# Kernel optimization log

Measured on AMD Instinct MI355X. Metric: run time of the kernel, lower is better.

The kernel has to match this reference:

```python
import jax, jax.numpy as jnp
import numpy as np

AGENT = 0
TAU = 0.5
EPS = 1e-10


def setup_inputs() -> dict:
    key = jax.random.key(0)
    ks = jax.random.split(key, 8)
    B, A, L, D, AD, OUT = 32768, 6, 225, 128, 64, 5
    E = A - 1  # 5 visible entities
    return {
        "observation": jax.random.normal(ks[0], (B, A, L), dtype=jnp.float32),
        "enc_w": jax.random.normal(ks[1], (L, D), dtype=jnp.float32) * 0.05,
        "enc_b": jnp.zeros((D,), dtype=jnp.float32),
        "q_w": jax.random.normal(ks[2], (D, AD), dtype=jnp.float32) * 0.05,
        "k_w": jax.random.normal(ks[3], (D, AD), dtype=jnp.float32) * 0.05,
        "fc_w": jax.random.normal(ks[4], (2 * E * D, OUT), dtype=jnp.float32) * 0.05,
        "fc_b": jnp.zeros((OUT,), dtype=jnp.float32),
        "u": jax.random.uniform(ks[5], (B, OUT), dtype=jnp.float32),
    }


def reference(observation, enc_w, enc_b, q_w, k_w, fc_w, fc_b, u):
    B, A, L = observation.shape
    others = np.array([i for i in range(A) if i != AGENT])  # static index list
    vis_obs = observation[:, others]          # (B, E, L)
    ag_obs = observation[:, AGENT:AGENT + 1]  # (B, 1, L)

    # ObservationEncoder: Linear + ReLU (shared weights)
    ag_e = jax.nn.relu(ag_obs @ enc_w + enc_b)    # (B, 1, D)
    vis_e = jax.nn.relu(vis_obs @ enc_w + enc_b)  # (B, E, D)

    # EntityAttention: scaled dot-product, softmax over entities
    q = ag_e @ q_w   # (B, 1, AD)
    k = vis_e @ k_w  # (B, E, AD)
    scores = jnp.einsum('bqa,bea->be', q, k) / jnp.sqrt(jnp.asarray(q.shape[-1], q.dtype))
    alphas = jax.nn.softmax(scores, axis=-1)  # (B, E)

    # attention-weighted per-entity encodings
    weighted = alphas[..., None] * vis_e                      # (B, E, D)
    agent_rep = jnp.broadcast_to(ag_e, weighted.shape)        # (B, E, D)
    concat = jnp.concatenate([agent_rep, weighted], axis=-2)  # (B, 2E, D)
    flat = concat.reshape(B, -1)                              # (B, 2*E*D)

    logits = flat @ fc_w + fc_b  # (B, OUT)

    # gumbel_softmax(tau=0.5, hard=False)
    g = -jnp.log(-jnp.log(u + EPS) + EPS)
    probs = jax.nn.softmax((logits + g) / TAU, axis=1)
    predicted_actions = jnp.argmax(probs, axis=1, keepdims=True)  # (B, 1) int
    return predicted_actions
```

## Files before the change

kernel.cpp:

```cpp
#include <hip/hip_runtime.h>
#include <math.h>

#define NB   32768
#define AG   6
#define LL   225
#define DD   128
#define EE   5
#define NOUT 5
#define ADIM 64

#define WS_M        0
#define WS_W1T      16384
#define WS_F2T      17024
#define WS_BSWZ_B   80896

#define SBLK 16
#define ENC_STRIDE 132
#define LDS_FLOATS 12672

typedef __attribute__((ext_vector_type(8))) short short8v;
typedef __attribute__((ext_vector_type(4))) float float4v;

__device__ __forceinline__ unsigned short bf_hi(float x, float* rem) {
    unsigned u = __float_as_uint(x);
    unsigned r = (u + 0x7FFFu + ((u >> 16) & 1u)) & 0xFFFF0000u;
    *rem = x - __uint_as_float(r);
    return (unsigned short)(r >> 16);
}

struct Tri { unsigned h, m, l; };
__device__ __forceinline__ Tri split2(float x0, float x1) {
    Tri t;
    unsigned u0 = __float_as_uint(x0), u1 = __float_as_uint(x1);
    t.h = __builtin_amdgcn_perm(u1, u0, 0x07060302u);
    float r0 = x0 - __uint_as_float(u0 & 0xFFFF0000u);
    float r1 = x1 - __uint_as_float(u1 & 0xFFFF0000u);
    unsigned v0 = __float_as_uint(r0), v1 = __float_as_uint(r1);
    t.m = __builtin_amdgcn_perm(v1, v0, 0x07060302u);
    float q0 = r0 - __uint_as_float(v0 & 0xFFFF0000u);
    float q1 = r1 - __uint_as_float(v1 & 0xFFFF0000u);
    t.l = __builtin_amdgcn_perm(__float_as_uint(q1), __float_as_uint(q0), 0x07060302u);
    return t;
}

__device__ __forceinline__ void stage8(unsigned short* aswz, const float* obs_blk,
                                       int slot, int k0) {
    const int r  = slot >> 3;
    const int k8 = slot & 7;
    const int k  = k0 + 8 * k8;
    float4 v0 = make_float4(0.f, 0.f, 0.f, 0.f);
    float4 v1 = make_float4(0.f, 0.f, 0.f, 0.f);
    if (k + 7 <= 224) {
        v0 = *(const float4*)&obs_blk[r * LL + k];
        v1 = *(const float4*)&obs_blk[r * LL + k + 4];
    } else if (k == 224) {
        v0.x = obs_blk[r * LL + 224];
    }
    Tri a = split2(v0.x, v0.y);
    Tri b = split2(v0.z, v0.w);
    Tri cc = split2(v1.x, v1.y);
    Tri d = split2(v1.z, v1.w);
    const int mt  = r >> 4, mm = r & 15;
    const int kbL = k8 >> 2;
    const int la  = mm + 16 * (k8 & 3);
    const int pla = la ^ ((la >> 2) & 12);
    unsigned short* p = aswz + ((kbL * 6 + mt) * 3) * 512 + pla * 8;
    *(uint4*)(p)        = make_uint4(a.h, b.h, cc.h, d.h);
    *(uint4*)(p + 512)  = make_uint4(a.m, b.m, cc.m, d.m);
    *(uint4*)(p + 1024) = make_uint4(a.l, b.l, cc.l, d.l);
}

__global__ void precompute_kernel(const float* __restrict__ q_w,
                                  const float* __restrict__ k_w,
                                  const float* __restrict__ enc_w,
                                  const float* __restrict__ fc_w,
                                  float* __restrict__ ws) {
    int b = blockIdx.x;
    int t = threadIdx.x;
    if (b < 128) {
        float s = 0.f;
        #pragma unroll 8
        for (int j = 0; j < ADIM; ++j)
            s = fmaf(q_w[b * ADIM + j], k_w[t * ADIM + j], s);
        ws[WS_M + b * 128 + t] = s * 0.125f;
    } else if (b == 128) {
        int d = t;
        #pragma unroll
        for (int o = 0; o < NOUT; ++o) {
            float s = 0.f;
            #pragma unroll
            for (int e = 0; e < EE; ++e)
                s += fc_w[(e * 128 + d) * NOUT + o];
            ws[WS_W1T + o * 128 + d] = s;
            #pragma unroll
            for (int e = 0; e < EE; ++e)
                ws[WS_F2T + (e * 5 + o) * 128 + d] = fc_w[(640 + e * 128 + d) * NOUT + o];
        }
    } else {
        int idx = (b - 129) * 128 + t;
        int lane = idx & 63;
        int rest = idx >> 6;
        int s    = rest % 3;
        int r2   = rest / 3;
        int nt   = r2 & 7;
        int kb   = r2 >> 3;
        unsigned short* bs = (unsigned short*)((char*)ws + WS_BSWZ_B);
        const int n     = nt * 16 + (lane & 15);
        const int kbase = kb * 32 + (lane >> 4) * 8;
        #pragma unroll
        for (int j = 0; j < 8; ++j) {
            int k = kbase + j;
            float x = (k < LL) ? enc_w[k * DD + n] : 0.f;
            float q1, q2, q3;
            unsigned short h = bf_hi(x,  &q1);
            unsigned short m = bf_hi(q1, &q2);
            unsigned short l = bf_hi(q2, &q3);
            bs[(((kb * 8 + nt) * 3 + s) * 64 + lane) * 8 + j] =
                (s == 0) ? h : (s == 1) ? m : l;
        }
    }
}

__global__ __launch_bounds__(512, 4)
void policy_kernel(const float* __restrict__ obs,
                   const float* __restrict__ enc_b,
                   const float* __restrict__ fc_b,
                   const float* __restrict__ u,
                   const float* __restrict__ ws,
                   int* __restrict__ out) {
    __shared__ float lds[LDS_FLOATS];
    unsigned short* aswz = (unsigned short*)lds;

    const int tid  = threadIdx.x;
    const int lane = tid & 63;
    const int w    = tid >> 6;
    const int wr   = w >> 2;
    const int wc   = w & 3;
    const int bs0  = blockIdx.x * SBLK;
    const float* obs_blk = obs + (size_t)bs0 * (AG * LL);
    const unsigned short* bswz = (const unsigned short*)((const char*)ws + WS_BSWZ_B);
    const int pl8 = (lane ^ ((lane >> 2) & 12)) * 8;

    float4v acc[3][2];
    #pragma unroll
    for (int m3 = 0; m3 < 3; ++m3)
        #pragma unroll
        for (int nt = 0; nt < 2; ++nt)
            acc[m3][nt] = (float4v){0.f, 0.f, 0.f, 0.f};

    #pragma unroll 1
    for (int c = 0; c < 4; ++c) {
        const int k0 = 64 * c;
        stage8(aswz, obs_blk, tid, k0);
        if (tid < 256) stage8(aswz, obs_blk, 512 + tid, k0);
        __syncthreads();

        #pragma unroll
        for (int kbL = 0; kbL < 2; ++kbL) {
            const int kb = 2 * c + kbL;
            short8v Bf[2][3];
            #pragma unroll
            for (int nt = 0; nt < 2; ++nt)
                #pragma unroll
                for (int s = 0; s < 3; ++s)
                    Bf[nt][s] = *(const short8v*)
                        &bswz[(((kb * 8 + (2 * wc + nt)) * 3 + s) * 64 + lane) * 8];
            #pragma unroll
            for (int m3 = 0; m3 < 3; ++m3) {
                const unsigned short* ap =
                    aswz + ((kbL * 6 + (wr * 3 + m3)) * 3) * 512 + pl8;
                short8v Ah = *(const short8v*)(ap);
                short8v Am = *(const short8v*)(ap + 512);
                short8v Al = *(const short8v*)(ap + 1024);
                #pragma unroll
                for (int nt = 0; nt < 2; ++nt) {
                    float4v d = acc[m3][nt];
                    d = __builtin_amdgcn_mfma_f32_16x16x32_bf16(Ah, Bf[nt][0], d, 0, 0, 0);
                    d = __builtin_amdgcn_mfma_f32_16x16x32_bf16(Ah, Bf[nt][1], d, 0, 0, 0);
                    d = __builtin_amdgcn_mfma_f32_16x16x32_bf16(Am, Bf[nt][0], d, 0, 0, 0);
                    d = __builtin_amdgcn_mfma_f32_16x16x32_bf16(Ah, Bf[nt][2], d, 0, 0, 0);
                    d = __builtin_amdgcn_mfma_f32_16x16x32_bf16(Al, Bf[nt][0], d, 0, 0, 0);
                    d = __builtin_amdgcn_mfma_f32_16x16x32_bf16(Am, Bf[nt][1], d, 0, 0, 0);
                    acc[m3][nt] = d;
                }
            }
        }
        __syncthreads();
    }

    {
        #pragma unroll
        for (int nt = 0; nt < 2; ++nt) {
            const int col = (2 * wc + nt) * 16 + (lane & 15);
            const float bb = enc_b[col];
            #pragma unroll
            for (int m3 = 0; m3 < 3; ++m3) {
                const int rbase = (wr * 3 + m3) * 16 + (lane >> 4) * 4;
                #pragma unroll
                for (int reg = 0; reg < 4; ++reg)
                    lds[(rbase + reg) * ENC_STRIDE + col] =
                        fmaxf(acc[m3][nt][reg] + bb, 0.f);
            }
        }
    }
    __syncthreads();

    const float* Mw = ws + WS_M;
    const int c0 = 2 * lane;
    const int sA = 2 * w;
    const int rA = sA * AG;
    const int rB = rA + AG;

    float t0[2] = {0.f, 0.f}, t1[2] = {0.f, 0.f};
    #pragma unroll 4
    for (int d = 0; d < DD; d += 4) {
        float4 a0 = *(const float4*)&lds[rA * ENC_STRIDE + d];
        float4 a1 = *(const float4*)&lds[rB * ENC_STRIDE + d];
        float2 m0 = *(const float2*)&Mw[(size_t)(d + 0) * DD + c0];
        float2 m1 = *(const float2*)&Mw[(size_t)(d + 1) * DD + c0];
        float2 m2 = *(const float2*)&Mw[(size_t)(d + 2) * DD + c0];
        float2 m3 = *(const float2*)&Mw[(size_t)(d + 3) * DD + c0];
        t0[0] = fmaf(a0.x, m0.x, t0[0]); t1[0] = fmaf(a0.x, m0.y, t1[0]);
        t0[0] = fmaf(a0.y, m1.x, t0[0]); t1[0] = fmaf(a0.y, m1.y, t1[0]);
        t0[0] = fmaf(a0.z, m2.x, t0[0]); t1[0] = fmaf(a0.z, m2.y, t1[0]);
        t0[0] = fmaf(a0.w, m3.x, t0[0]); t1[0] = fmaf(a0.w, m3.y, t1[0]);
        t0[1] = fmaf(a1.x, m0.x, t0[1]); t1[1] = fmaf(a1.x, m0.y, t1[1]);
        t0[1] = fmaf(a1.y, m1.x, t0[1]); t1[1] = fmaf(a1.y, m1.y, t1[1]);
        t0[1] = fmaf(a1.z, m2.x, t0[1]); t1[1] = fmaf(a1.z, m2.y, t1[1]);
        t0[1] = fmaf(a1.w, m3.x, t0[1]); t1[1] = fmaf(a1.w, m3.y, t1[1]);
    }

    float vx[2][EE], vy[2][EE], sc[2][EE];
    #pragma unroll
    for (int j = 0; j < 2; ++j)
        #pragma unroll
        for (int e = 0; e < EE; ++e) {
            float2 v = *(const float2*)&lds[((sA + j) * AG + 1 + e) * ENC_STRIDE + c0];
            vx[j][e] = v.x; vy[j][e] = v.y;
            sc[j][e] = t0[j] * v.x + t1[j] * v.y;
        }
    #pragma unroll
    for (int off = 32; off > 0; off >>= 1)
        #pragma unroll
        for (int j = 0; j < 2; ++j)
            #pragma unroll
            for (int e = 0; e < EE; ++e)
                sc[j][e] += __shfl_xor(sc[j][e], off, 64);

    float alpha[2][EE];
    #pragma unroll
    for (int j = 0; j < 2; ++j) {
        float mx = sc[j][0];
        #pragma unroll
        for (int e = 1; e < EE; ++e) mx = fmaxf(mx, sc[j][e]);
        float sum = 0.f;
        #pragma unroll
        for (int e = 0; e < EE; ++e) { alpha[j][e] = expf(sc[j][e] - mx); sum += alpha[j][e]; }
        const float inv = 1.f / sum;
        #pragma unroll
        for (int e = 0; e < EE; ++e) alpha[j][e] *= inv;
    }

    float Lg[2][NOUT];
    #pragma unroll
    for (int j = 0; j < 2; ++j) {
        float2 a2 = *(const float2*)&lds[(sA + j) * AG * ENC_STRIDE + c0];
        #pragma unroll
        for (int o = 0; o < NOUT; ++o) {
            float2 w1 = *(const float2*)&ws[WS_W1T + o * DD + c0];
            Lg[j][o] = fmaf(a2.x, w1.x, a2.y * w1.y);
        }
    }
    #pragma unroll
    for (int e = 0; e < EE; ++e) {
        float wxj[2], wyj[2];
        #pragma unroll
        for (int j = 0; j < 2; ++j) { wxj[j] = alpha[j][e] * vx[j][e]; wyj[j] = alpha[j][e] * vy[j][e]; }
        #pragma unroll
        for (int o = 0; o < NOUT; ++o) {
            float2 f2 = *(const float2*)&ws[WS_F2T + (e * NOUT + o) * DD + c0];
            #pragma unroll
            for (int j = 0; j < 2; ++j)
                Lg[j][o] = fmaf(wxj[j], f2.x, fmaf(wyj[j], f2.y, Lg[j][o]));
        }
    }
    #pragma unroll
    for (int off = 32; off > 0; off >>= 1)
        #pragma unroll
        for (int j = 0; j < 2; ++j)
            #pragma unroll
            for (int o = 0; o < NOUT; ++o)
                Lg[j][o] += __shfl_xor(Lg[j][o], off, 64);

    const int S0 = bs0 + sA;
    float y = -1e30f;
    if (lane < 10) {
        const int jl = lane / 5, ol = lane - 5 * jl;
        const float uu  = u[(size_t)S0 * NOUT + lane];
        const float gmb = -logf(-logf(uu + 1e-10f) + 1e-10f);
        y = Lg[jl][ol] + fc_b[ol] + gmb;
    }
    float b0 = -1e30f, b1 = -1e30f; int bi0 = 0, bi1 = 0;
    #pragma unroll
    for (int o = 0; o < NOUT; ++o) {
        float y0 = __shfl(y, o, 64);
        float y1 = __shfl(y, 5 + o, 64);
        if (y0 > b0) { b0 = y0; bi0 = o; }
        if (y1 > b1) { b1 = y1; bi1 = o; }
    }
    if (lane < 2) out[S0 + lane] = lane ? bi1 : bi0;
}

extern "C" void kernel_launch(void* const* d_in, const int* in_sizes, int n_in,
                              void* d_out, int out_size, void* d_ws, size_t ws_size,
                              hipStream_t stream) {
    const float* obs   = (const float*)d_in[0];
    const float* enc_w = (const float*)d_in[1];
    const float* enc_b = (const float*)d_in[2];
    const float* q_w   = (const float*)d_in[3];
    const float* k_w   = (const float*)d_in[4];
    const float* fc_w  = (const float*)d_in[5];
    const float* fc_b  = (const float*)d_in[6];
    const float* uu    = (const float*)d_in[7];
    float* ws = (float*)d_ws;
    int*   po = (int*)d_out;

    precompute_kernel<<<225, 128, 0, stream>>>(q_w, k_w, enc_w, fc_w, ws);
    policy_kernel<<<NB / SBLK, 512, 0, stream>>>(obs, enc_b, fc_b, uu, ws, po);
}
```

Baseline: 366.7 us.

## Load A fragments directly from global into registers, dropping LDS staging

Each wave now reads its own observation rows from global memory straight into MFMA A-fragment registers and does the bf16 triple split there, instead of staging the split tiles through LDS. This removes the LDS writes and reads and the two barriers per K chunk. In exchange, each A row is loaded redundantly by the four column waves, using fewer coalesced per-lane reads. Launch bounds drop to 2 blocks per CU and the LDS array shrinks to the epilogue size.

Result: slower. 414.9 us (+13.2%).

```diff
diff --git a/kernel.cpp b/kernel.cpp
--- a/kernel.cpp
+++ b/kernel.cpp
@@ -16,7 +16,7 @@
 
 #define SBLK 16
 #define ENC_STRIDE 132
-#define LDS_FLOATS 12672
+#define LDS_FLOATS (96 * ENC_STRIDE)
 
 typedef __attribute__((ext_vector_type(8))) short short8v;
 typedef __attribute__((ext_vector_type(4))) float float4v;
@@ -43,31 +43,18 @@
     return t;
 }
 
-__device__ __forceinline__ void stage8(unsigned short* aswz, const float* obs_blk,
-                                       int slot, int k0) {
-    const int r  = slot >> 3;
-    const int k8 = slot & 7;
-    const int k  = k0 + 8 * k8;
-    float4 v0 = make_float4(0.f, 0.f, 0.f, 0.f);
-    float4 v1 = make_float4(0.f, 0.f, 0.f, 0.f);
-    if (k + 7 <= 224) {
-        v0 = *(const float4*)&obs_blk[r * LL + k];
-        v1 = *(const float4*)&obs_blk[r * LL + k + 4];
-    } else if (k == 224) {
-        v0.x = obs_blk[r * LL + 224];
-    }
+__device__ __forceinline__ void splitA(const float4& v0, const float4& v1,
+                                       short8v* Ah, short8v* Am, short8v* Al) {
     Tri a = split2(v0.x, v0.y);
     Tri b = split2(v0.z, v0.w);
-    Tri cc = split2(v1.x, v1.y);
+    Tri c = split2(v1.x, v1.y);
     Tri d = split2(v1.z, v1.w);
-    const int mt  = r >> 4, mm = r & 15;
-    const int kbL = k8 >> 2;
-    const int la  = mm + 16 * (k8 & 3);
-    const int pla = la ^ ((la >> 2) & 12);
-    unsigned short* p = aswz + ((kbL * 6 + mt) * 3) * 512 + pla * 8;
-    *(uint4*)(p)        = make_uint4(a.h, b.h, cc.h, d.h);
-    *(uint4*)(p + 512)  = make_uint4(a.m, b.m, cc.m, d.m);
-    *(uint4*)(p + 1024) = make_uint4(a.l, b.l, cc.l, d.l);
+    uint4 H = make_uint4(a.h, b.h, c.h, d.h);
+    uint4 M = make_uint4(a.m, b.m, c.m, d.m);
+    uint4 L = make_uint4(a.l, b.l, c.l, d.l);
+    *Ah = *(short8v*)&H;
+    *Am = *(short8v*)&M;
+    *Al = *(short8v*)&L;
 }
 
 __global__ void precompute_kernel(const float* __restrict__ q_w,
@@ -121,7 +108,7 @@
     }
 }
 
-__global__ __launch_bounds__(512, 4)
+__global__ __launch_bounds__(512, 2)
 void policy_kernel(const float* __restrict__ obs,
                    const float* __restrict__ enc_b,
                    const float* __restrict__ fc_b,
@@ -129,7 +116,6 @@
                    const float* __restrict__ ws,
                    int* __restrict__ out) {
     __shared__ float lds[LDS_FLOATS];
-    unsigned short* aswz = (unsigned short*)lds;
 
     const int tid  = threadIdx.x;
     const int lane = tid & 63;
@@ -139,7 +125,6 @@
     const int bs0  = blockIdx.x * SBLK;
     const float* obs_blk = obs + (size_t)bs0 * (AG * LL);
     const unsigned short* bswz = (const unsigned short*)((const char*)ws + WS_BSWZ_B);
-    const int pl8 = (lane ^ ((lane >> 2) & 12)) * 8;
 
     float4v acc[3][2];
     #pragma unroll
@@ -148,44 +133,56 @@
         for (int nt = 0; nt < 2; ++nt)
             acc[m3][nt] = (float4v){0.f, 0.f, 0.f, 0.f};
 
+    const int rlo = lane & 15;
+    const int kg  = lane >> 4;
+    const float* rp0 = obs_blk + (size_t)((wr * 3 + 0) * 16 + rlo) * LL;
+    const float* rp1 = obs_blk + (size_t)((wr * 3 + 1) * 16 + rlo) * LL;
+    const float* rp2 = obs_blk + (size_t)((wr * 3 + 2) * 16 + rlo) * LL;
+
     #pragma unroll 1
-    for (int c = 0; c < 4; ++c) {
-        const int k0 = 64 * c;
-        stage8(aswz, obs_blk, tid, k0);
-        if (tid < 256) stage8(aswz, obs_blk, 512 + tid, k0);
-        __syncthreads();
-
-        #pragma unroll
-        for (int kbL = 0; kbL < 2; ++kbL) {
-            const int kb = 2 * c + kbL;
-            short8v Bf[2][3];
-            #pragma unroll
-            for (int nt = 0; nt < 2; ++nt)
-                #pragma unroll
-                for (int s = 0; s < 3; ++s)
-                    Bf[nt][s] = *(const short8v*)
-                        &bswz[(((kb * 8 + (2 * wc + nt)) * 3 + s) * 64 + lane) * 8];
-            #pragma unroll
-            for (int m3 = 0; m3 < 3; ++m3) {
-                const unsigned short* ap =
-                    aswz + ((kbL * 6 + (wr * 3 + m3)) * 3) * 512 + pl8;
-                short8v Ah = *(const short8v*)(ap);
-                short8v Am = *(const short8v*)(ap + 512);
-                short8v Al = *(const short8v*)(ap + 1024);
-                #pragma unroll
-                for (int nt = 0; nt < 2; ++nt) {
-                    float4v d = acc[m3][nt];
-                    d = __builtin_amdgcn_mfma_f32_16x16x32_bf16(Ah, Bf[nt][0], d, 0, 0, 0);
-                    d = __builtin_amdgcn_mfma_f32_16x16x32_bf16(Ah, Bf[nt][1], d, 0, 0, 0);
-                    d = __builtin_amdgcn_mfma_f32_16x16x32_bf16(Am, Bf[nt][0], d, 0, 0, 0);
-                    d = __builtin_amdgcn_mfma_f32_16x16x32_bf16(Ah, Bf[nt][2], d, 0, 0, 0);
-                    d = __builtin_amdgcn_mfma_f32_16x16x32_bf16(Al, Bf[nt][0], d, 0, 0, 0);
-                    d = __builtin_amdgcn_mfma_f32_16x16x32_bf16(Am, Bf[nt][1], d, 0, 0, 0);
-                    acc[m3][nt] = d;
-                }
+    for (int kb = 0; kb < 8; ++kb) {
+        short8v Bf[2][3];
+        #pragma unroll
+        for (int nt = 0; nt < 2; ++nt)
+            #pragma unroll
+            for (int s = 0; s < 3; ++s)
+                Bf[nt][s] = *(const short8v*)
+                    &bswz[(((kb * 8 + (2 * wc + nt)) * 3 + s) * 64 + lane) * 8];
+
+        float4 va[3][2];
+        if (kb < 7) {
+            const int k = kb * 32 + kg * 8;
+            va[0][0] = *(const float4*)(rp0 + k);
+            va[0][1] = *(const float4*)(rp0 + k + 4);
+            va[1][0] = *(const float4*)(rp1 + k);
+            va[1][1] = *(const float4*)(rp1 + k + 4);
+            va[2][0] = *(const float4*)(rp2 + k);
+            va[2][1] = *(const float4*)(rp2 + k + 4);
+        } else {
+            va[0][0] = make_float4(kg == 0 ? rp0[224] : 0.f, 0.f, 0.f, 0.f);
+            va[1][0] = make_float4(kg == 0 ? rp1[224] : 0.f, 0.f, 0.f, 0.f);
+            va[2][0] = make_float4(kg == 0 ? rp2[224] : 0.f, 0.f, 0.f, 0.f);
+            va[0][1] = make_float4(0.f, 0.f, 0.f, 0.f);
+            va[1][1] = make_float4(0.f, 0.f, 0.f, 0.f);
+            va[2][1] = make_float4(0.f, 0.f, 0.f, 0.f);
+        }
+
+        #pragma unroll
+        for (int m3 = 0; m3 < 3; ++m3) {
+            short8v Ah, Am, Al;
+            splitA(va[m3][0], va[m3][1], &Ah, &Am, &Al);
+            #pragma unroll
+            for (int nt = 0; nt < 2; ++nt) {
+                float4v d = acc[m3][nt];
+                d = __builtin_amdgcn_mfma_f32_16x16x32_bf16(Ah, Bf[nt][0], d, 0, 0, 0);
+                d = __builtin_amdgcn_mfma_f32_16x16x32_bf16(Ah, Bf[nt][1], d, 0, 0, 0);
+                d = __builtin_amdgcn_mfma_f32_16x16x32_bf16(Am, Bf[nt][0], d, 0, 0, 0);
+                d = __builtin_amdgcn_mfma_f32_16x16x32_bf16(Ah, Bf[nt][2], d, 0, 0, 0);
+                d = __builtin_amdgcn_mfma_f32_16x16x32_bf16(Al, Bf[nt][0], d, 0, 0, 0);
+                d = __builtin_amdgcn_mfma_f32_16x16x32_bf16(Am, Bf[nt][1], d, 0, 0, 0);
+                acc[m3][nt] = d;
             }
         }
-        __syncthreads();
     }
 
     {
```

## Halve block size and prefetch next observation chunk into registers during MFMA

Applied to the files above, without the earlier changes.

Shrinks each block from 16 to 8 samples (48 rows, 4 waves, 256 threads) so more blocks fit per CU, with a matching LDS size and swizzle. The observation load for the next K chunk is issued into registers before the MFMA work on the current chunk, and split and stored to LDS at the start of the next iteration, overlapping global latency with compute. B fragments are now loaded per nt inside the loop. The smaller block means each wave does more B-fragment global loads per sample and runs more blocks in total.

After: 548.5 us. 1.5x slower.

```diff
diff --git a/kernel.cpp b/kernel.cpp
--- a/kernel.cpp
+++ b/kernel.cpp
@@ -14,9 +14,9 @@
 #define WS_F2T      17024
 #define WS_BSWZ_B   80896
 
-#define SBLK 16
+#define SBLK 8
 #define ENC_STRIDE 132
-#define LDS_FLOATS 12672
+#define LDS_FLOATS (48 * ENC_STRIDE)
 
 typedef __attribute__((ext_vector_type(8))) short short8v;
 typedef __attribute__((ext_vector_type(4))) float float4v;
@@ -41,33 +41,6 @@
     float q1 = r1 - __uint_as_float(v1 & 0xFFFF0000u);
     t.l = __builtin_amdgcn_perm(__float_as_uint(q1), __float_as_uint(q0), 0x07060302u);
     return t;
-}
-
-__device__ __forceinline__ void stage8(unsigned short* aswz, const float* obs_blk,
-                                       int slot, int k0) {
-    const int r  = slot >> 3;
-    const int k8 = slot & 7;
-    const int k  = k0 + 8 * k8;
-    float4 v0 = make_float4(0.f, 0.f, 0.f, 0.f);
-    float4 v1 = make_float4(0.f, 0.f, 0.f, 0.f);
-    if (k + 7 <= 224) {
-        v0 = *(const float4*)&obs_blk[r * LL + k];
-        v1 = *(const float4*)&obs_blk[r * LL + k + 4];
-    } else if (k == 224) {
-        v0.x = obs_blk[r * LL + 224];
-    }
-    Tri a = split2(v0.x, v0.y);
-    Tri b = split2(v0.z, v0.w);
-    Tri cc = split2(v1.x, v1.y);
-    Tri d = split2(v1.z, v1.w);
-    const int mt  = r >> 4, mm = r & 15;
-    const int kbL = k8 >> 2;
-    const int la  = mm + 16 * (k8 & 3);
-    const int pla = la ^ ((la >> 2) & 12);
-    unsigned short* p = aswz + ((kbL * 6 + mt) * 3) * 512 + pla * 8;
-    *(uint4*)(p)        = make_uint4(a.h, b.h, cc.h, d.h);
-    *(uint4*)(p + 512)  = make_uint4(a.m, b.m, cc.m, d.m);
-    *(uint4*)(p + 1024) = make_uint4(a.l, b.l, cc.l, d.l);
 }
 
 __global__ void precompute_kernel(const float* __restrict__ q_w,
@@ -121,7 +94,35 @@
     }
 }
 
-__global__ __launch_bounds__(512, 4)
+#define LOADSEG(prow, k, v0, v1)                                             \
+    do {                                                                     \
+        v0 = make_float4(0.f, 0.f, 0.f, 0.f);                                \
+        v1 = make_float4(0.f, 0.f, 0.f, 0.f);                                \
+        if ((k) + 7 <= 224) {                                                \
+            v0 = *(const float4*)((prow) + (k));                             \
+            v1 = *(const float4*)((prow) + (k) + 4);                         \
+        } else if ((k) == 224) {                                             \
+            v0.x = (prow)[224];                                              \
+        }                                                                    \
+    } while (0)
+
+#define STORESEG(v0, v1, r, k8)                                              \
+    do {                                                                     \
+        Tri t0 = split2((v0).x, (v0).y);                                     \
+        Tri t1 = split2((v0).z, (v0).w);                                     \
+        Tri t2 = split2((v1).x, (v1).y);                                     \
+        Tri t3 = split2((v1).z, (v1).w);                                     \
+        const int mt  = (r) >> 4;                                            \
+        const int kbL = (k8) >> 2;                                           \
+        const int la  = ((r) & 15) + 16 * ((k8) & 3);                        \
+        const int pla = la ^ ((la >> 3) & 6);                                \
+        unsigned short* p = aswz + ((kbL * 3 + mt) * 3) * 512 + pla * 8;     \
+        *(uint4*)(p)        = make_uint4(t0.h, t1.h, t2.h, t3.h);            \
+        *(uint4*)(p + 512)  = make_uint4(t0.m, t1.m, t2.m, t3.m);            \
+        *(uint4*)(p + 1024) = make_uint4(t0.l, t1.l, t2.l, t3.l);            \
+    } while (0)
+
+__global__ __launch_bounds__(256, 6)
 void policy_kernel(const float* __restrict__ obs,
                    const float* __restrict__ enc_b,
                    const float* __restrict__ fc_b,
@@ -134,12 +135,17 @@
     const int tid  = threadIdx.x;
     const int lane = tid & 63;
     const int w    = tid >> 6;
-    const int wr   = w >> 2;
-    const int wc   = w & 3;
     const int bs0  = blockIdx.x * SBLK;
     const float* obs_blk = obs + (size_t)bs0 * (AG * LL);
     const unsigned short* bswz = (const unsigned short*)((const char*)ws + WS_BSWZ_B);
-    const int pl8 = (lane ^ ((lane >> 2) & 12)) * 8;
+    const int pl8 = (lane ^ ((lane >> 3) & 6)) * 8;
+
+    const int rS  = tid >> 3;
+    const int k8  = tid & 7;
+    const bool hasB = (tid < 128);
+    const int rS2 = 32 + (tid >> 3);
+    const float* prowA = obs_blk + rS  * LL;
+    const float* prowB = obs_blk + rS2 * LL;
 
     float4v acc[3][2];
     #pragma unroll
@@ -148,54 +154,65 @@
         for (int nt = 0; nt < 2; ++nt)
             acc[m3][nt] = (float4v){0.f, 0.f, 0.f, 0.f};
 
+    float4 a0, a1, b0, b1;
+    {
+        const int k = 8 * k8;
+        LOADSEG(prowA, k, a0, a1);
+        if (hasB) LOADSEG(prowB, k, b0, b1);
+    }
+
     #pragma unroll 1
     for (int c = 0; c < 4; ++c) {
-        const int k0 = 64 * c;
-        stage8(aswz, obs_blk, tid, k0);
-        if (tid < 256) stage8(aswz, obs_blk, 512 + tid, k0);
+        if (c) __syncthreads();
+        STORESEG(a0, a1, rS, k8);
+        if (hasB) STORESEG(b0, b1, rS2, k8);
+        if (c < 3) {
+            const int k = 64 * (c + 1) + 8 * k8;
+            LOADSEG(prowA, k, a0, a1);
+            if (hasB) LOADSEG(prowB, k, b0, b1);
+        }
         __syncthreads();
 
         #pragma unroll
         for (int kbL = 0; kbL < 2; ++kbL) {
             const int kb = 2 * c + kbL;
-            short8v Bf[2][3];
-            #pragma unroll
-            for (int nt = 0; nt < 2; ++nt)
+            #pragma unroll
+            for (int nt = 0; nt < 2; ++nt) {
+                short8v Bs0 = *(const short8v*)
+                    &bswz[(((kb * 8 + (2 * w + nt)) * 3 + 0) * 64 + lane) * 8];
+                short8v Bs1 = *(const short8v*)
+                    &bswz[(((kb * 8 + (2 * w + nt)) * 3 + 1) * 64 + lane) * 8];
+                short8v Bs2 = *(const short8v*)
+                    &bswz[(((kb * 8 + (2 * w + nt)) * 3 + 2) * 64 + lane) * 8];
                 #pragma unroll
-                for (int s = 0; s < 3; ++s)
-                    Bf[nt][s] = *(const short8v*)
-                        &bswz[(((kb * 8 + (2 * wc + nt)) * 3 + s) * 64 + lane) * 8];
-            #pragma unroll
-            for (int m3 = 0; m3 < 3; ++m3) {
-                const unsigned short* ap =
-                    aswz + ((kbL * 6 + (wr * 3 + m3)) * 3) * 512 + pl8;
-                short8v Ah = *(const short8v*)(ap);
-                short8v Am = *(const short8v*)(ap + 512);
-                short8v Al = *(const short8v*)(ap + 1024);
-                #pragma unroll
-                for (int nt = 0; nt < 2; ++nt) {
+                for (int m3 = 0; m3 < 3; ++m3) {
+                    const unsigned short* ap =
+                        aswz + ((kbL * 3 + m3) * 3) * 512 + pl8;
+                    short8v Ah = *(const short8v*)(ap);
+                    short8v Am = *(const short8v*)(ap + 512);
+                    short8v Al = *(const short8v*)(ap + 1024);
                     float4v d = acc[m3][nt];
-                    d = __builtin_amdgcn_mfma_f32_16x16x32_bf16(Ah, Bf[nt][0], d, 0, 0, 0);
-                    d = __builtin_amdgcn_mfma_f32_16x16x32_bf16(Ah, Bf[nt][1], d, 0, 0, 0);
-                    d = __builtin_amdgcn_mfma_f32_16x16x32_bf16(Am, Bf[nt][0], d, 0, 0, 0);
-                    d = __builtin_amdgcn_mfma_f32_16x16x32_bf16(Ah, Bf[nt][2], d, 0, 0, 0);
-                    d = __builtin_amdgcn_mfma_f32_16x16x32_bf16(Al, Bf[nt][0], d, 0, 0, 0);
-                    d = __builtin_amdgcn_mfma_f32_16x16x32_bf16(Am, Bf[nt][1], d, 0, 0, 0);
+                    d = __builtin_amdgcn_mfma_f32_16x16x32_bf16(Ah, Bs0, d, 0, 0, 0);
+                    d = __builtin_amdgcn_mfma_f32_16x16x32_bf16(Ah, Bs1, d, 0, 0, 0);
+                    d = __builtin_amdgcn_mfma_f32_16x16x32_bf16(Am, Bs0, d, 0, 0, 0);
+                    d = __builtin_amdgcn_mfma_f32_16x16x32_bf16(Ah, Bs2, d, 0, 0, 0);
+                    d = __builtin_amdgcn_mfma_f32_16x16x32_bf16(Al, Bs0, d, 0, 0, 0);
+                    d = __builtin_amdgcn_mfma_f32_16x16x32_bf16(Am, Bs1, d, 0, 0, 0);
                     acc[m3][nt] = d;
                 }
             }
         }
-        __syncthreads();
-    }
+    }
+    __syncthreads();
 
     {
         #pragma unroll
         for (int nt = 0; nt < 2; ++nt) {
-            const int col = (2 * wc + nt) * 16 + (lane & 15);
+            const int col = (2 * w + nt) * 16 + (lane & 15);
             const float bb = enc_b[col];
             #pragma unroll
             for (int m3 = 0; m3 < 3; ++m3) {
-                const int rbase = (wr * 3 + m3) * 16 + (lane >> 4) * 4;
+                const int rbase = m3 * 16 + (lane >> 4) * 4;
                 #pragma unroll
                 for (int reg = 0; reg < 4; ++reg)
                     lds[(rbase + reg) * ENC_STRIDE + col] =
@@ -214,20 +231,20 @@
     float t0[2] = {0.f, 0.f}, t1[2] = {0.f, 0.f};
     #pragma unroll 4
     for (int d = 0; d < DD; d += 4) {
-        float4 a0 = *(const float4*)&lds[rA * ENC_STRIDE + d];
-        float4 a1 = *(const float4*)&lds[rB * ENC_STRIDE + d];
+        float4 a0v = *(const float4*)&lds[rA * ENC_STRIDE + d];
+        float4 a1v = *(const float4*)&lds[rB * ENC_STRIDE + d];
         float2 m0 = *(const float2*)&Mw[(size_t)(d + 0) * DD + c0];
         float2 m1 = *(const float2*)&Mw[(size_t)(d + 1) * DD + c0];
         float2 m2 = *(const float2*)&Mw[(size_t)(d + 2) * DD + c0];
         float2 m3 = *(const float2*)&Mw[(size_t)(d + 3) * DD + c0];
-        t0[0] = fmaf(a0.x, m0.x, t0[0]); t1[0] = fmaf(a0.x, m0.y, t1[0]);
-        t0[0] = fmaf(a0.y, m1.x, t0[0]); t1[0] = fmaf(a0.y, m1.y, t1[0]);
-        t0[0] = fmaf(a0.z, m2.x, t0[0]); t1[0] = fmaf(a0.z, m2.y, t1[0]);
-        t0[0] = fmaf(a0.w, m3.x, t0[0]); t1[0] = fmaf(a0.w, m3.y, t1[0]);
-        t0[1] = fmaf(a1.x, m0.x, t0[1]); t1[1] = fmaf(a1.x, m0.y, t1[1]);
-        t0[1] = fmaf(a1.y, m1.x, t0[1]); t1[1] = fmaf(a1.y, m1.y, t1[1]);
-        t0[1] = fmaf(a1.z, m2.x, t0[1]); t1[1] = fmaf(a1.z, m2.y, t1[1]);
-        t0[1] = fmaf(a1.w, m3.x, t0[1]); t1[1] = fmaf(a1.w, m3.y, t1[1]);
+        t0[0] = fmaf(a0v.x, m0.x, t0[0]); t1[0] = fmaf(a0v.x, m0.y, t1[0]);
+        t0[0] = fmaf(a0v.y, m1.x, t0[0]); t1[0] = fmaf(a0v.y, m1.y, t1[0]);
+        t0[0] = fmaf(a0v.z, m2.x, t0[0]); t1[0] = fmaf(a0v.z, m2.y, t1[0]);
+        t0[0] = fmaf(a0v.w, m3.x, t0[0]); t1[0] = fmaf(a0v.w, m3.y, t1[0]);
+        t0[1] = fmaf(a1v.x, m0.x, t0[1]); t1[1] = fmaf(a1v.x, m0.y, t1[1]);
+        t0[1] = fmaf(a1v.y, m1.x, t0[1]); t1[1] = fmaf(a1v.y, m1.y, t1[1]);
+        t0[1] = fmaf(a1v.z, m2.x, t0[1]); t1[1] = fmaf(a1v.z, m2.y, t1[1]);
+        t0[1] = fmaf(a1v.w, m3.x, t0[1]); t1[1] = fmaf(a1v.w, m3.y, t1[1]);
     }
 
     float vx[2][EE], vy[2][EE], sc[2][EE];
@@ -300,13 +317,13 @@
         const float gmb = -logf(-logf(uu + 1e-10f) + 1e-10f);
         y = Lg[jl][ol] + fc_b[ol] + gmb;
     }
-    float b0 = -1e30f, b1 = -1e30f; int bi0 = 0, bi1 = 0;
+    float p0 = -1e30f, p1 = -1e30f; int bi0 = 0, bi1 = 0;
     #pragma unroll
     for (int o = 0; o < NOUT; ++o) {
         float y0 = __shfl(y, o, 64);
         float y1 = __shfl(y, 5 + o, 64);
-        if (y0 > b0) { b0 = y0; bi0 = o; }
-        if (y1 > b1) { b1 = y1; bi1 = o; }
+        if (y0 > p0) { p0 = y0; bi0 = o; }
+        if (y1 > p1) { p1 = y1; bi1 = o; }
     }
     if (lane < 2) out[S0 + lane] = lane ? bi1 : bi0;
 }
@@ -326,5 +343,5 @@
     int*   po = (int*)d_out;
 
     precompute_kernel<<<225, 128, 0, stream>>>(q_w, k_w, enc_w, fc_w, ws);
-    policy_kernel<<<NB / SBLK, 512, 0, stream>>>(obs, enc_b, fc_b, uu, ws, po);
-}
+    policy_kernel<<<NB / SBLK, 256, 0, stream>>>(obs, enc_b, fc_b, uu, ws, po);
+}
```
